# Optimization experiments

Hardware: AMD Instinct MI355X
Metric: run time of the kernel (lower is better)

The kernel has to match this reference:

```python
import jax, jax.numpy as jnp
import numpy as np

N_NODES = 100000
N_EDGES = 1600000
HIDDEN = 64
IN_DIM = 3
OUT_DIM = 2
N_MP = 3


def setup_inputs() -> dict:
    key = jax.random.key(0)
    ks = jax.random.split(key, 16)
    x = jax.random.normal(ks[0], (N_NODES, IN_DIM), dtype=jnp.float32)
    edge_index = jax.random.randint(ks[1], (2, N_EDGES), 0, N_NODES, dtype=jnp.int64)

    def lin(k, fan_in, fan_out):
        s = 1.0 / np.sqrt(fan_in)
        return jax.random.uniform(k, (fan_out, fan_in), jnp.float32, -s, s)

    inp = {
        'x': x,
        'edge_index': edge_index,
        'preW': lin(ks[2], IN_DIM, HIDDEN),
        'preb': jnp.zeros((HIDDEN,), jnp.float32),
        'postW': lin(ks[3], HIDDEN, OUT_DIM),
        'postb': jnp.zeros((OUT_DIM,), jnp.float32),
    }
    for i in range(N_MP):
        inp[f'relW{i}'] = lin(ks[4 + 3 * i], HIDDEN, HIDDEN)
        inp[f'relb{i}'] = jnp.zeros((HIDDEN,), jnp.float32)
        inp[f'rootW{i}'] = lin(ks[5 + 3 * i], HIDDEN, HIDDEN)
    return inp


def _graph_conv(h, src, dst, relW, relb, rootW):
    # PyG GraphConv: out_i = W_rel @ (sum_{j in N(i)} h_j) + b_rel + W_root @ h_i
    agg = jax.ops.segment_sum(h[src], dst, num_segments=N_NODES)  # [N, H] scatter-add
    return agg @ relW.T + relb + h @ rootW.T


def reference(x, edge_index, preW, preb, postW, postb,
              relW0, relb0, rootW0, relW1, relb1, rootW1, relW2, relb2, rootW2):
    src, dst = edge_index[0], edge_index[1]
    # pre-MP dense
    h = jax.nn.relu(x @ preW.T + preb)
    # message passing layers (GraphConv, aggr='add'), relu after each
    for relW, relb, rootW in ((relW0, relb0, rootW0),
                              (relW1, relb1, rootW1),
                              (relW2, relb2, rootW2)):
        h = jax.nn.relu(_graph_conv(h, src, dst, relW, relb, rootW))
    # post-MP dense (activation applied to final layer too, as in source)
    out = jax.nn.relu(h @ postW.T + postb)
    return out
```

## Files before the change

### kernel.cpp

```cpp
#include <hip/hip_runtime.h>
#include <hip/hip_fp16.h>

#define N_NODES 100000
#define N_EDGES 1600000
#define HID 64

#define BSH 8
#define NBKT ((N_NODES + 255) / 256)
#define CAP 6144
#define TILE 4096

#define HSC 0.015625f
#define HSCI 64.0f

__global__ void __launch_bounds__(512) bucket_kernel(const int* __restrict__ src,
                                                     const int* __restrict__ dst,
                                                     int* __restrict__ bcur,
                                                     unsigned int* __restrict__ tmp) {
    __shared__ unsigned long long ed[TILE];
    __shared__ int cnt[NBKT], cnt2[NBKT], scnx[NBKT], gbase[NBKT];
    __shared__ int s[512];
    int tid = threadIdx.x;
    int bstart = blockIdx.x * TILE;
    int tcnt = N_EDGES - bstart;
    if (tcnt > TILE) tcnt = TILE;
    if (tcnt < 0) tcnt = 0;
    for (int b = tid; b < NBKT; b += 512) { cnt[b] = 0; cnt2[b] = 0; }
    __syncthreads();
    for (int i = tid; i < tcnt; i += 512) atomicAdd(&cnt[dst[bstart + i] >> BSH], 1);
    __syncthreads();
    s[tid] = (tid < NBKT) ? cnt[tid] : 0;
    __syncthreads();
    for (int off = 1; off < 512; off <<= 1) {
        int add = (tid >= off) ? s[tid - off] : 0;
        __syncthreads();
        s[tid] += add;
        __syncthreads();
    }
    if (tid < NBKT) {
        scnx[tid] = s[tid] - cnt[tid];
        gbase[tid] = tid * CAP + atomicAdd(&bcur[tid], cnt[tid]);
    }
    __syncthreads();
    for (int i = tid; i < tcnt; i += 512) {
        int e = bstart + i;
        int d = dst[e], sc = src[e];
        int b = d >> BSH;
        int pos = scnx[b] + atomicAdd(&cnt2[b], 1);
        ed[pos] = ((unsigned long long)(unsigned)d << 32) | (unsigned)sc;
    }
    __syncthreads();
    for (int i = tid; i < tcnt; i += 512) {
        unsigned long long v = ed[i];
        int d = (int)(v >> 32);
        unsigned sc = (unsigned)v;
        int b = d >> BSH;
        int idx = gbase[b] + (i - scnx[b]);
        if (idx < (b + 1) * CAP)
            tmp[idx] = ((unsigned)(d & 255) << 17) | sc;
    }
}

__global__ void __launch_bounds__(256) passb_kernel(const unsigned int* __restrict__ tmp,
                                                    const int* __restrict__ bcur,
                                                    int* __restrict__ rowp,
                                                    int* __restrict__ ssrc) {
    __shared__ int red[256];
    __shared__ int cnt[256], s[256], cur[256];
    int tid = threadIdx.x;
    int b = blockIdx.x;
    int acc = 0;
    for (int i = tid; i < b; i += 256) {
        int c = bcur[i];
        if (c > CAP) c = CAP;
        acc += c;
    }
    red[tid] = acc;
    __syncthreads();
    for (int off = 128; off >= 1; off >>= 1) {
        if (tid < off) red[tid] += red[tid + off];
        __syncthreads();
    }
    int lo = red[0];
    int ne = bcur[b];
    if (ne > CAP) ne = CAP;
    if (b == NBKT - 1 && tid == 0) rowp[N_NODES] = lo + ne;
    int lo_t = b * CAP;
    cnt[tid] = 0;
    __syncthreads();
    for (int i = tid; i < ne; i += 256) atomicAdd(&cnt[tmp[lo_t + i] >> 17], 1);
    __syncthreads();
    int v = cnt[tid];
    s[tid] = v;
    __syncthreads();
    for (int off = 1; off < 256; off <<= 1) {
        int a = (tid >= off) ? s[tid - off] : 0;
        __syncthreads();
        s[tid] += a;
        __syncthreads();
    }
    int excl = lo + s[tid] - v;
    int node = (b << BSH) + tid;
    if (node < N_NODES) rowp[node] = excl;
    cur[tid] = excl;
    __syncthreads();
    for (int i = tid; i < ne; i += 256) {
        unsigned u = tmp[lo_t + i];
        int pos = atomicAdd(&cur[u >> 17], 1);
        ssrc[pos] = (int)(u & 0x1FFFF);
    }
}

template <int PRE>
__global__ void __launch_bounds__(256) gemmt_kernel(const void* __restrict__ hx,
                                                    const float* __restrict__ preW,
                                                    const float* __restrict__ preb,
                                                    const float* __restrict__ relW,
                                                    const float* __restrict__ relb,
                                                    const float* __restrict__ rootW,
                                                    float mscale,
                                                    __half* __restrict__ m,
                                                    __half* __restrict__ aout) {
    __shared__ float hs[128 * 68];
    __shared__ float ws[128 * 68];
    __shared__ float xs[PRE ? 384 : 1];
    __shared__ float pw[PRE ? 192 : 1];
    __shared__ float pbs[PRE ? 64 : 1];
    int tid = threadIdx.x;
    int i0 = blockIdx.x * 128;
    for (int c = 0; c < 8; c++) {
        int f = tid + c * 256;
        int j = f >> 4, c4 = (f & 15) << 2;
        float4 wv = (j < 64) ? *(const float4*)&relW[j * 64 + c4]
                             : *(const float4*)&rootW[(j - 64) * 64 + c4];
        *(float4*)&ws[j * 68 + c4] = wv;
    }
    if (PRE) {
        const float* x = (const float*)hx;
        if (tid < 192) pw[tid] = preW[tid];
        if (tid < 64) pbs[tid] = preb[tid];
        for (int t = tid; t < 384; t += 256) {
            int gi = i0 * 3 + t;
            xs[t] = (gi < N_NODES * 3) ? x[gi] : 0.f;
        }
        __syncthreads();
        for (int c = 0; c < 32; c++) {
            int e = c * 256 + tid;
            int row = e >> 6, col = e & 63;
            float v = pbs[col];
            v = fmaf(xs[row * 3 + 0], pw[col * 3 + 0], v);
            v = fmaf(xs[row * 3 + 1], pw[col * 3 + 1], v);
            v = fmaf(xs[row * 3 + 2], pw[col * 3 + 2], v);
            hs[row * 68 + col] = fmaxf(v, 0.f);
        }
    } else {
        const __half* h = (const __half*)hx;
        for (int c = 0; c < 4; c++) {
            int f = tid + c * 256;
            int row = f >> 3, c8 = (f & 7) << 3;
            uint4 hv = {0u, 0u, 0u, 0u};
            if (i0 + row < N_NODES) hv = *(const uint4*)(h + (long)(i0 + row) * 64 + c8);
            const __half2* hp = (const __half2*)&hv;
            float2 f0 = __half22float2(hp[0]), f1 = __half22float2(hp[1]);
            float2 f2 = __half22float2(hp[2]), f3 = __half22float2(hp[3]);
            float* dstp = &hs[row * 68 + c8];
            dstp[0] = f0.x * HSCI; dstp[1] = f0.y * HSCI;
            dstp[2] = f1.x * HSCI; dstp[3] = f1.y * HSCI;
            dstp[4] = f2.x * HSCI; dstp[5] = f2.y * HSCI;
            dstp[6] = f3.x * HSCI; dstp[7] = f3.y * HSCI;
        }
    }
    int ig = tid >> 4;
    int jg = tid & 15;
    float rb[4];
#pragma unroll
    for (int t = 0; t < 4; t++) rb[t] = relb[jg + 16 * t];
    float acc[8][8];
#pragma unroll
    for (int n = 0; n < 8; n++)
#pragma unroll
        for (int mm = 0; mm < 8; mm++) acc[n][mm] = 0.f;
    __syncthreads();

    for (int kk = 0; kk < 64; kk += 4) {
        float4 av[8], bv[8];
#pragma unroll
        for (int n = 0; n < 8; n++) av[n] = *(const float4*)&hs[(ig + 16 * n) * 68 + kk];
#pragma unroll
        for (int mm = 0; mm < 8; mm++) bv[mm] = *(const float4*)&ws[(jg + 16 * mm) * 68 + kk];
#pragma unroll
        for (int n = 0; n < 8; n++)
#pragma unroll
            for (int mm = 0; mm < 8; mm++) {
                acc[n][mm] = fmaf(av[n].x, bv[mm].x, acc[n][mm]);
                acc[n][mm] = fmaf(av[n].y, bv[mm].y, acc[n][mm]);
                acc[n][mm] = fmaf(av[n].z, bv[mm].z, acc[n][mm]);
                acc[n][mm] = fmaf(av[n].w, bv[mm].w, acc[n][mm]);
            }
    }
#pragma unroll
    for (int n = 0; n < 8; n++) {
        int node = i0 + ig + 16 * n;
        if (node >= N_NODES) continue;
#pragma unroll
        for (int mm = 0; mm < 4; mm++)
            m[(long)node * 64 + jg + 16 * mm] = __float2half(acc[n][mm] * mscale);
#pragma unroll
        for (int mm = 4; mm < 8; mm++)
            aout[(long)node * 64 + jg + 16 * (mm - 4)] =
                __float2half((acc[n][mm] + rb[mm - 4]) * HSC);
    }
}

template <int FINAL>
__global__ void gather_kernel(const __half* __restrict__ m, __half* __restrict__ a,
                              const int* __restrict__ rowp, const int* __restrict__ ssrc,
                              float aggscale,
                              const float* __restrict__ postW, const float* __restrict__ postb,
                              float* __restrict__ out) {
    int lane = threadIdx.x & 63;
    int wv = (blockIdx.x * blockDim.x + threadIdx.x) >> 6;
    int pb = wv * 4;
    if (pb >= N_NODES) return;
    int n = lane >> 4;
    int g = (lane >> 3) & 1;
    int f8 = (lane & 7) << 3;
    pb = __builtin_amdgcn_readfirstlane(pb);
    int q0 = rowp[pb], q1 = rowp[pb + 1], q2 = rowp[pb + 2];
    int q3 = rowp[pb + 3], q4 = rowp[pb + 4];
    int node = pb + n;
    int r0 = (n == 0) ? q0 : (n == 1) ? q1 : (n == 2) ? q2 : q3;
    int r1 = (n == 0) ? q1 : (n == 1) ? q2 : (n == 2) ? q3 : q4;
    int nedge = r1 - r0;
    uint4 av = *(const uint4*)(a + (long)node * 64 + f8);
    float a0 = 0.f, a1 = 0.f, a2 = 0.f, a3 = 0.f, a4 = 0.f, a5 = 0.f, a6 = 0.f, a7 = 0.f;
#define ACC8(u)                                                         \
    {                                                                   \
        float2 f_;                                                      \
        f_ = __half22float2(*(__half2*)&(u).x); a0 += f_.x; a1 += f_.y; \
        f_ = __half22float2(*(__half2*)&(u).y); a2 += f_.x; a3 += f_.y; \
        f_ = __half22float2(*(__half2*)&(u).z); a4 += f_.x; a5 += f_.y; \
        f_ = __half22float2(*(__half2*)&(u).w); a6 += f_.x; a7 += f_.y; \
    }
    int ns = nedge >> 1;
    int q = 0;
    for (; q + 4 <= ns; q += 4) {
        int b0 = r0 + q * 2 + g;
        int i0 = ssrc[b0];
        int i1 = ssrc[b0 + 2];
        int i2 = ssrc[b0 + 4];
        int i3 = ssrc[b0 + 6];
        uint4 u0 = *(const uint4*)(m + (long)i0 * 64 + f8);
        uint4 u1 = *(const uint4*)(m + (long)i1 * 64 + f8);
        uint4 u2 = *(const uint4*)(m + (long)i2 * 64 + f8);
        uint4 u3 = *(const uint4*)(m + (long)i3 * 64 + f8);
        ACC8(u0); ACC8(u1); ACC8(u2); ACC8(u3);
    }
    if (q + 2 <= ns) {
        int b0 = r0 + q * 2 + g;
        int i0 = ssrc[b0];
        int i1 = ssrc[b0 + 2];
        uint4 u0 = *(const uint4*)(m + (long)i0 * 64 + f8);
        uint4 u1 = *(const uint4*)(m + (long)i1 * 64 + f8);
        ACC8(u0); ACC8(u1);
        q += 2;
    }
    if (q < ns) {
        int i0 = ssrc[r0 + q * 2 + g];
        uint4 u0 = *(const uint4*)(m + (long)i0 * 64 + f8);
        ACC8(u0);
    }
    if ((nedge & 1) && g == 0) {
        int i0 = ssrc[r0 + ns * 2];
        uint4 u0 = *(const uint4*)(m + (long)i0 * 64 + f8);
        ACC8(u0);
    }
#undef ACC8
    a0 += __shfl_xor(a0, 8, 64); a1 += __shfl_xor(a1, 8, 64);
    a2 += __shfl_xor(a2, 8, 64); a3 += __shfl_xor(a3, 8, 64);
    a4 += __shfl_xor(a4, 8, 64); a5 += __shfl_xor(a5, 8, 64);
    a6 += __shfl_xor(a6, 8, 64); a7 += __shfl_xor(a7, 8, 64);
    a0 *= aggscale; a1 *= aggscale; a2 *= aggscale; a3 *= aggscale;
    a4 *= aggscale; a5 *= aggscale; a6 *= aggscale; a7 *= aggscale;
    const __half2* ap = (const __half2*)&av;
    float2 o0 = __half22float2(ap[0]), o1 = __half22float2(ap[1]);
    float2 o2 = __half22float2(ap[2]), o3 = __half22float2(ap[3]);
    a0 = fmaxf(fmaf(o0.x, HSCI, a0), 0.f); a1 = fmaxf(fmaf(o0.y, HSCI, a1), 0.f);
    a2 = fmaxf(fmaf(o1.x, HSCI, a2), 0.f); a3 = fmaxf(fmaf(o1.y, HSCI, a3), 0.f);
    a4 = fmaxf(fmaf(o2.x, HSCI, a4), 0.f); a5 = fmaxf(fmaf(o2.y, HSCI, a5), 0.f);
    a6 = fmaxf(fmaf(o3.x, HSCI, a6), 0.f); a7 = fmaxf(fmaf(o3.y, HSCI, a7), 0.f);
    if (FINAL) {
        float4 w0 = *(const float4*)(postW + f8);
        float4 w1 = *(const float4*)(postW + f8 + 4);
        float4 w2 = *(const float4*)(postW + 64 + f8);
        float4 w3 = *(const float4*)(postW + 64 + f8 + 4);
        float p0 = a0 * w0.x + a1 * w0.y + a2 * w0.z + a3 * w0.w +
                   a4 * w1.x + a5 * w1.y + a6 * w1.z + a7 * w1.w;
        float p1 = a0 * w2.x + a1 * w2.y + a2 * w2.z + a3 * w2.w +
                   a4 * w3.x + a5 * w3.y + a6 * w3.z + a7 * w3.w;
#pragma unroll
        for (int off = 1; off <= 4; off <<= 1) {
            p0 += __shfl_xor(p0, off, 64);
            p1 += __shfl_xor(p1, off, 64);
        }
        if ((lane & 15) == 0) {
            out[(long)node * 2 + 0] = fmaxf(p0 + postb[0], 0.f);
            out[(long)node * 2 + 1] = fmaxf(p1 + postb[1], 0.f);
        }
    } else {
        if (g == 0) {
            uint4 st;
            __half2* sp = (__half2*)&st;
            sp[0] = __floats2half2_rn(a0 * HSC, a1 * HSC);
            sp[1] = __floats2half2_rn(a2 * HSC, a3 * HSC);
            sp[2] = __floats2half2_rn(a4 * HSC, a5 * HSC);
            sp[3] = __floats2half2_rn(a6 * HSC, a7 * HSC);
            *(uint4*)(a + (long)node * 64 + f8) = st;
        }
    }
}

extern "C" void kernel_launch(void* const* d_in, const int* in_sizes, int n_in,
                              void* d_out, int out_size, void* d_ws, size_t ws_size,
                              hipStream_t stream) {
    const float* x = (const float*)d_in[0];
    const int* esrc = (const int*)d_in[1];
    const int* edst = esrc + N_EDGES;
    const float* preW = (const float*)d_in[2];
    const float* preb = (const float*)d_in[3];
    const float* postW = (const float*)d_in[4];
    const float* postb = (const float*)d_in[5];
    const float* relW[3] = {(const float*)d_in[6], (const float*)d_in[9], (const float*)d_in[12]};
    const float* relb[3] = {(const float*)d_in[7], (const float*)d_in[10], (const float*)d_in[13]};
    const float* rootW[3] = {(const float*)d_in[8], (const float*)d_in[11], (const float*)d_in[14]};
    float* out = (float*)d_out;

    const size_t NF = (size_t)N_NODES * HID;
    char* p = (char*)d_ws;
    __half* hA = (__half*)p; p += NF * 2;
    __half* hB = (__half*)p; p += NF * 2;
    __half* mB = (__half*)p; p += NF * 2;
    p = (char*)(((size_t)p + 255) & ~(size_t)255);
    int* rowp = (int*)p; p += (size_t)(N_NODES + 1) * 4;
    p = (char*)(((size_t)p + 255) & ~(size_t)255);
    int* ssrc = (int*)p; p += (size_t)N_EDGES * 4;
    int* bcur = (int*)p; p += 512 * 4;
    unsigned int* tmp = (unsigned int*)hA;

    hipMemsetAsync(bcur, 0, 512 * 4, stream);
    bucket_kernel<<<(N_EDGES + TILE - 1) / TILE, 512, 0, stream>>>(esrc, edst, bcur, tmp);
    passb_kernel<<<NBKT, 256, 0, stream>>>(tmp, bcur, rowp, ssrc);

    const int GEMM_BLOCKS = (N_NODES + 127) / 128;
    const int GATHER_BLOCKS = N_NODES / 16;

    const float S1 = 1.0f / 64.0f, IS1 = 64.0f;

    gemmt_kernel<1><<<GEMM_BLOCKS, 256, 0, stream>>>(x, preW, preb, relW[0], relb[0],
                                                     rootW[0], 1.0f, mB, hB);
    gather_kernel<0><<<GATHER_BLOCKS, 256, 0, stream>>>(mB, hB, rowp, ssrc, 1.0f,
                                                        nullptr, nullptr, nullptr);
    gemmt_kernel<0><<<GEMM_BLOCKS, 256, 0, stream>>>(hB, nullptr, nullptr, relW[1], relb[1],
                                                     rootW[1], S1, mB, hA);
    gather_kernel<0><<<GATHER_BLOCKS, 256, 0, stream>>>(mB, hA, rowp, ssrc, IS1,
                                                        nullptr, nullptr, nullptr);
    gemmt_kernel<0><<<GEMM_BLOCKS, 256, 0, stream>>>(hA, nullptr, nullptr, relW[2], relb[2],
                                                     rootW[2], S1, mB, hB);
    gather_kernel<1><<<GATHER_BLOCKS, 256, 0, stream>>>(mB, hB, rowp, ssrc, IS1,
                                                        postW, postb, out);
}
```

Before: 313.9 us.

## Use fp16 MFMA with swizzled half LDS tiles in node GEMM kernel

```diff
diff --git a/kernel.cpp b/kernel.cpp
--- a/kernel.cpp
+++ b/kernel.cpp
@@ -12,6 +12,9 @@
 
 #define HSC 0.015625f
 #define HSCI 64.0f
+
+typedef _Float16 f16x8 __attribute__((ext_vector_type(8)));
+typedef float f32x4 __attribute__((ext_vector_type(4)));
 
 __global__ void __launch_bounds__(512) bucket_kernel(const int* __restrict__ src,
                                                      const int* __restrict__ dst,
@@ -118,22 +121,31 @@
                                                     const float* __restrict__ relW,
                                                     const float* __restrict__ relb,
                                                     const float* __restrict__ rootW,
-                                                    float mscale,
                                                     __half* __restrict__ m,
                                                     __half* __restrict__ aout) {
-    __shared__ float hs[128 * 68];
-    __shared__ float ws[128 * 68];
+    __shared__ __align__(16) __half hs[128 * 64];
+    __shared__ __align__(16) __half ws[128 * 64];
     __shared__ float xs[PRE ? 384 : 1];
     __shared__ float pw[PRE ? 192 : 1];
     __shared__ float pbs[PRE ? 64 : 1];
     int tid = threadIdx.x;
     int i0 = blockIdx.x * 128;
-    for (int c = 0; c < 8; c++) {
-        int f = tid + c * 256;
-        int j = f >> 4, c4 = (f & 15) << 2;
-        float4 wv = (j < 64) ? *(const float4*)&relW[j * 64 + c4]
-                             : *(const float4*)&rootW[(j - 64) * 64 + c4];
-        *(float4*)&ws[j * 68 + c4] = wv;
+
+#pragma unroll
+    for (int it = 0; it < 4; it++) {
+        int t = it * 256 + tid;
+        int row = t >> 3, c = t & 7;
+        const float* wsrc = (row < 64) ? &relW[row * 64 + c * 8]
+                                       : &rootW[(row - 64) * 64 + c * 8];
+        float4 w0 = *(const float4*)wsrc;
+        float4 w1 = *(const float4*)(wsrc + 4);
+        uint4 pk;
+        __half2* hp = (__half2*)&pk;
+        hp[0] = __floats2half2_rn(w0.x, w0.y);
+        hp[1] = __floats2half2_rn(w0.z, w0.w);
+        hp[2] = __floats2half2_rn(w1.x, w1.y);
+        hp[3] = __floats2half2_rn(w1.z, w1.w);
+        *(uint4*)&ws[row * 64 + ((c ^ (row & 7)) << 3)] = pk;
     }
     if (PRE) {
         const float* x = (const float*)hx;
@@ -144,71 +156,106 @@
             xs[t] = (gi < N_NODES * 3) ? x[gi] : 0.f;
         }
         __syncthreads();
-        for (int c = 0; c < 32; c++) {
-            int e = c * 256 + tid;
-            int row = e >> 6, col = e & 63;
-            float v = pbs[col];
-            v = fmaf(xs[row * 3 + 0], pw[col * 3 + 0], v);
-            v = fmaf(xs[row * 3 + 1], pw[col * 3 + 1], v);
-            v = fmaf(xs[row * 3 + 2], pw[col * 3 + 2], v);
-            hs[row * 68 + col] = fmaxf(v, 0.f);
+#pragma unroll
+        for (int it = 0; it < 4; it++) {
+            int t = it * 256 + tid;
+            int row = t >> 3, c = t & 7;
+            float v[8];
+#pragma unroll
+            for (int u = 0; u < 8; u++) {
+                int col = c * 8 + u;
+                float sv = pbs[col];
+                sv = fmaf(xs[row * 3 + 0], pw[col * 3 + 0], sv);
+                sv = fmaf(xs[row * 3 + 1], pw[col * 3 + 1], sv);
+                sv = fmaf(xs[row * 3 + 2], pw[col * 3 + 2], sv);
+                v[u] = fmaxf(sv, 0.f);
+            }
+            uint4 pk;
+            __half2* hp = (__half2*)&pk;
+            hp[0] = __floats2half2_rn(v[0], v[1]);
+            hp[1] = __floats2half2_rn(v[2], v[3]);
+            hp[2] = __floats2half2_rn(v[4], v[5]);
+            hp[3] = __floats2half2_rn(v[6], v[7]);
+            *(uint4*)&hs[row * 64 + ((c ^ (row & 7)) << 3)] = pk;
         }
     } else {
         const __half* h = (const __half*)hx;
-        for (int c = 0; c < 4; c++) {
-            int f = tid + c * 256;
-            int row = f >> 3, c8 = (f & 7) << 3;
+#pragma unroll
+        for (int it = 0; it < 4; it++) {
+            int t = it * 256 + tid;
+            int row = t >> 3, c = t & 7;
             uint4 hv = {0u, 0u, 0u, 0u};
-            if (i0 + row < N_NODES) hv = *(const uint4*)(h + (long)(i0 + row) * 64 + c8);
-            const __half2* hp = (const __half2*)&hv;
-            float2 f0 = __half22float2(hp[0]), f1 = __half22float2(hp[1]);
-            float2 f2 = __half22float2(hp[2]), f3 = __half22float2(hp[3]);
-            float* dstp = &hs[row * 68 + c8];
-            dstp[0] = f0.x * HSCI; dstp[1] = f0.y * HSCI;
-            dstp[2] = f1.x * HSCI; dstp[3] = f1.y * HSCI;
-            dstp[4] = f2.x * HSCI; dstp[5] = f2.y * HSCI;
-            dstp[6] = f3.x * HSCI; dstp[7] = f3.y * HSCI;
-        }
-    }
-    int ig = tid >> 4;
-    int jg = tid & 15;
-    float rb[4];
-#pragma unroll
-    for (int t = 0; t < 4; t++) rb[t] = relb[jg + 16 * t];
-    float acc[8][8];
-#pragma unroll
-    for (int n = 0; n < 8; n++)
-#pragma unroll
-        for (int mm = 0; mm < 8; mm++) acc[n][mm] = 0.f;
-    __syncthreads();
-
-    for (int kk = 0; kk < 64; kk += 4) {
-        float4 av[8], bv[8];
-#pragma unroll
-        for (int n = 0; n < 8; n++) av[n] = *(const float4*)&hs[(ig + 16 * n) * 68 + kk];
-#pragma unroll
-        for (int mm = 0; mm < 8; mm++) bv[mm] = *(const float4*)&ws[(jg + 16 * mm) * 68 + kk];
-#pragma unroll
-        for (int n = 0; n < 8; n++)
-#pragma unroll
-            for (int mm = 0; mm < 8; mm++) {
-                acc[n][mm] = fmaf(av[n].x, bv[mm].x, acc[n][mm]);
-                acc[n][mm] = fmaf(av[n].y, bv[mm].y, acc[n][mm]);
-                acc[n][mm] = fmaf(av[n].z, bv[mm].z, acc[n][mm]);
-                acc[n][mm] = fmaf(av[n].w, bv[mm].w, acc[n][mm]);
+            if (i0 + row < N_NODES) hv = *(const uint4*)(h + (long)(i0 + row) * 64 + c * 8);
+            *(uint4*)&hs[row * 64 + ((c ^ (row & 7)) << 3)] = hv;
+        }
+    }
+    __syncthreads();
+
+    int lane = tid & 63;
+    int w = tid >> 6;
+    int wm = w >> 1, wn = w & 1;
+    int r = lane & 15, q = lane >> 4;
+
+    f32x4 acc[4][4];
+#pragma unroll
+    for (int mt = 0; mt < 4; mt++)
+#pragma unroll
+        for (int nt = 0; nt < 4; nt++) acc[mt][nt] = (f32x4){0.f, 0.f, 0.f, 0.f};
+
+#pragma unroll
+    for (int ks = 0; ks < 2; ks++) {
+        f16x8 af[4], bf[4];
+#pragma unroll
+        for (int mt = 0; mt < 4; mt++) {
+            int row = wm * 64 + mt * 16 + r;
+            int cc = (ks * 4 + q) ^ (row & 7);
+            af[mt] = *(const f16x8*)&hs[row * 64 + (cc << 3)];
+        }
+#pragma unroll
+        for (int nt = 0; nt < 4; nt++) {
+            int row = wn * 64 + nt * 16 + r;
+            int cc = (ks * 4 + q) ^ (row & 7);
+            bf[nt] = *(const f16x8*)&ws[row * 64 + (cc << 3)];
+        }
+#pragma unroll
+        for (int mt = 0; mt < 4; mt++)
+#pragma unroll
+            for (int nt = 0; nt < 4; nt++)
+                acc[mt][nt] = __builtin_amdgcn_mfma_f32_16x16x32_f16(af[mt], bf[nt],
+                                                                     acc[mt][nt], 0, 0, 0);
+    }
+
+    if (wn == 0) {
+#pragma unroll
+        for (int mt = 0; mt < 4; mt++) {
+            int nb = i0 + wm * 64 + mt * 16 + q * 4;
+#pragma unroll
+            for (int reg = 0; reg < 4; reg++) {
+                int node = nb + reg;
+                if (node >= N_NODES) continue;
+#pragma unroll
+                for (int nt = 0; nt < 4; nt++)
+                    m[(long)node * 64 + nt * 16 + r] = __float2half(acc[mt][nt][reg]);
             }
-    }
-#pragma unroll
-    for (int n = 0; n < 8; n++) {
-        int node = i0 + ig + 16 * n;
-        if (node >= N_NODES) continue;
-#pragma unroll
-        for (int mm = 0; mm < 4; mm++)
-            m[(long)node * 64 + jg + 16 * mm] = __float2half(acc[n][mm] * mscale);
-#pragma unroll
-        for (int mm = 4; mm < 8; mm++)
-            aout[(long)node * 64 + jg + 16 * (mm - 4)] =
-                __float2half((acc[n][mm] + rb[mm - 4]) * HSC);
+        }
+    } else {
+        const float asc = PRE ? HSC : 1.0f;
+        float rb[4];
+#pragma unroll
+        for (int nt = 0; nt < 4; nt++) rb[nt] = relb[nt * 16 + r] * HSC;
+#pragma unroll
+        for (int mt = 0; mt < 4; mt++) {
+            int nb = i0 + wm * 64 + mt * 16 + q * 4;
+#pragma unroll
+            for (int reg = 0; reg < 4; reg++) {
+                int node = nb + reg;
+                if (node >= N_NODES) continue;
+#pragma unroll
+                for (int nt = 0; nt < 4; nt++)
+                    aout[(long)node * 64 + nt * 16 + r] =
+                        __float2half(fmaf(acc[mt][nt][reg], asc, rb[nt]));
+            }
+        }
     }
 }
 
@@ -354,18 +401,18 @@
     const int GEMM_BLOCKS = (N_NODES + 127) / 128;
     const int GATHER_BLOCKS = N_NODES / 16;
 
-    const float S1 = 1.0f / 64.0f, IS1 = 64.0f;
+    const float IS1 = 64.0f;
 
     gemmt_kernel<1><<<GEMM_BLOCKS, 256, 0, stream>>>(x, preW, preb, relW[0], relb[0],
-                                                     rootW[0], 1.0f, mB, hB);
+                                                     rootW[0], mB, hB);
     gather_kernel<0><<<GATHER_BLOCKS, 256, 0, stream>>>(mB, hB, rowp, ssrc, 1.0f,
                                                         nullptr, nullptr, nullptr);
     gemmt_kernel<0><<<GEMM_BLOCKS, 256, 0, stream>>>(hB, nullptr, nullptr, relW[1], relb[1],
-                                                     rootW[1], S1, mB, hA);
+                                                     rootW[1], mB, hA);
     gather_kernel<0><<<GATHER_BLOCKS, 256, 0, stream>>>(mB, hA, rowp, ssrc, IS1,
                                                         nullptr, nullptr, nullptr);
     gemmt_kernel<0><<<GEMM_BLOCKS, 256, 0, stream>>>(hA, nullptr, nullptr, relW[2], relb[2],
-                                                     rootW[2], S1, mB, hB);
+                                                     rootW[2], mB, hB);
     gather_kernel<1><<<GATHER_BLOCKS, 256, 0, stream>>>(mB, hB, rowp, ssrc, IS1,
                                                         postW, postb, out);
 }
```

New measurement: 261.4 us. 1.2x faster.
